# Optimization experiments

Measured on AMD Instinct MI355X. Metric: run time of the kernel, lower is better.

## Reference

```python
import jax, jax.numpy as jnp
import numpy as np

B, N, C = 2, 2048, 1024
H = 16
D = C // H  # head_dim = 64

def setup_inputs() -> dict:
    key = jax.random.key(0)
    ks = jax.random.split(key, 5)
    scale = 1.0 / np.sqrt(C)
    return {
        "x": jax.random.normal(ks[0], (B, N, C), dtype=jnp.float32),
        "w_qkv": jax.random.normal(ks[1], (C, 3 * C), dtype=jnp.float32) * scale,
        "b_qkv": jnp.zeros((3 * C,), dtype=jnp.float32),
        "w_out": jax.random.normal(ks[2], (C, C), dtype=jnp.float32) * scale,
        "b_out": jnp.zeros((C,), dtype=jnp.float32),
    }

def reference(x, w_qkv, b_qkv, w_out, b_out):
    b, n, c = x.shape
    # fused QKV projection: [B,N,3C] -> [3,B,H,N,D]
    qkv = (x @ w_qkv + b_qkv).reshape(b, n, 3, H, D).transpose(2, 0, 3, 1, 4)
    q, k, v = qkv[0], qkv[1], qkv[2]
    # scaled dot-product attention (dropout is identity in eval / p=0)
    attn = jnp.einsum('bhqd,bhkd->bhqk', q, k) * (D ** -0.5)
    attn = jax.nn.softmax(attn, axis=-1)
    out = jnp.einsum('bhqk,bhkd->bhqd', attn, v)
    out = out.transpose(0, 2, 1, 3).reshape(b, n, c)
    return out @ w_out + b_out
```

## Files before the change

### kernel.cpp

```cpp
#include <hip/hip_runtime.h>

typedef unsigned short u16;
typedef __bf16 bf16x8 __attribute__((ext_vector_type(8)));
typedef __bf16 bf16x4 __attribute__((ext_vector_type(4)));
typedef float f32x4 __attribute__((ext_vector_type(4)));

#define LOG2E 1.44269504088896340736f

constexpr int Bc = 2, Nc = 2048, Cch = 1024, Hh = 16, Dd = 64;
constexpr int Mrows = Bc * Nc;
constexpr int N_QKV = 3 * Cch;

__device__ __forceinline__ u16 f2bf(float f) {
  unsigned int u = __float_as_uint(f);
  u += 0x7fffu + ((u >> 16) & 1u);
  return (u16)(u >> 16);
}

__device__ __forceinline__ void gload16(const void* g, void* l) {
  __builtin_amdgcn_global_load_lds((const __attribute__((address_space(1))) void*)g,
                                   (__attribute__((address_space(3))) void*)l, 16, 0, 0);
}

#define MFMA(a, b, c) __builtin_amdgcn_mfma_f32_16x16x32_bf16(a, b, c, 0, 0, 0)

__global__ __launch_bounds__(256) void cast_x_kernel(const float* __restrict__ in,
                                                     u16* __restrict__ out, int n4) {
  int i = blockIdx.x * 256 + threadIdx.x;
  if (i >= n4) return;
  float4 v = *(const float4*)&in[i * 4];
  union { u16 h[4]; short4 s; } u;
  u.h[0] = f2bf(v.x); u.h[1] = f2bf(v.y); u.h[2] = f2bf(v.z); u.h[3] = f2bf(v.w);
  *(short4*)&out[i * 4] = u.s;
}

__global__ __launch_bounds__(256) void transpose_cast_kernel(const float* __restrict__ in,
                                                             u16* __restrict__ out,
                                                             int R, int Cq) {
  __shared__ float tile[32][33];
  int bx = blockIdx.x * 32;
  int by = blockIdx.y * 32;
  int tx = threadIdx.x & 31, ty = threadIdx.x >> 5;
#pragma unroll
  for (int i = 0; i < 32; i += 8)
    tile[ty + i][tx] = in[(size_t)(by + ty + i) * Cq + bx + tx];
  __syncthreads();
#pragma unroll
  for (int i = 0; i < 32; i += 8)
    out[(size_t)(bx + ty + i) * R + by + tx] = f2bf(tile[tx][ty + i]);
}

__global__ __launch_bounds__(256) void gemm_qkv_kernel(const u16* __restrict__ A,
                                                       const u16* __restrict__ Bt,
                                                       const float* __restrict__ bias,
                                                       u16* __restrict__ Qo,
                                                       u16* __restrict__ Ko,
                                                       u16* __restrict__ Vto) {
  __shared__ u16 As[128 * 32];
  __shared__ u16 Bs[128 * 32];
  f32x4 acc[4][4] = {};
  int tid = threadIdx.x, lane = tid & 63, wid = tid >> 6;
  int wr = wid >> 1, wc = wid & 1;
  int l15 = lane & 15, g = lane >> 4;
  int rowBase = blockIdx.x * 128, colBase = blockIdx.y * 128;
  int rowS = tid >> 2, c8 = (tid & 3) << 3;

  for (int k0 = 0; k0 < 1024; k0 += 32) {
    __syncthreads();
    gload16(&A[(size_t)(rowBase + rowS) * 1024 + k0 + c8],        (char*)As + wid * 1024);
    gload16(&A[(size_t)(rowBase + 64 + rowS) * 1024 + k0 + c8],   (char*)As + 4096 + wid * 1024);
    gload16(&Bt[(size_t)(colBase + rowS) * 1024 + k0 + c8],       (char*)Bs + wid * 1024);
    gload16(&Bt[(size_t)(colBase + 64 + rowS) * 1024 + k0 + c8],  (char*)Bs + 4096 + wid * 1024);
    __syncthreads();
    bf16x8 af[4], bfv[4];
#pragma unroll
    for (int m = 0; m < 4; ++m)
      af[m] = *(const bf16x8*)&As[(wr * 64 + m * 16 + l15) * 32 + g * 8];
#pragma unroll
    for (int n = 0; n < 4; ++n)
      bfv[n] = *(const bf16x8*)&Bs[(wc * 64 + n * 16 + l15) * 32 + g * 8];
#pragma unroll
    for (int m = 0; m < 4; ++m)
#pragma unroll
      for (int n = 0; n < 4; ++n)
        acc[m][n] = MFMA(af[m], bfv[n], acc[m][n]);
  }

#pragma unroll
  for (int m = 0; m < 4; ++m)
#pragma unroll
    for (int n = 0; n < 4; ++n) {
      int colc = colBase + wc * 64 + n * 16 + l15;
      float bv = bias[colc];
      int s = colc >> 10, hd = colc & 1023;
      int h = hd >> 6, d = hd & 63;
      float scale = (s == 0) ? 0.125f : 1.0f;
#pragma unroll
      for (int j = 0; j < 4; ++j) {
        int r = rowBase + wr * 64 + m * 16 + g * 4 + j;
        int b = r >> 11, nn = r & 2047;
        u16 v = f2bf((acc[m][n][j] + bv) * scale);
        size_t bh = (size_t)(b * 16 + h);
        if (s == 0)      Qo[(bh * 2048 + nn) * 64 + d] = v;
        else if (s == 1) Ko[(bh * 2048 + nn) * 64 + d] = v;
        else             Vto[(bh * 64 + d) * 2048 + nn] = v;
      }
    }
}

__global__ __launch_bounds__(256) void attn_kernel(const u16* __restrict__ Q,
                                                   const u16* __restrict__ Km,
                                                   const u16* __restrict__ Vt,
                                                   u16* __restrict__ AO) {
  __shared__ u16 Ks[64 * 72];
  __shared__ u16 Vs[64 * 72];
  __shared__ u16 Ps[128 * 72];
  int tid = threadIdx.x, lane = tid & 63, w = tid >> 6;
  int l15 = lane & 15, g = lane >> 4;
  int bidw = (blockIdx.x & 7) * 64 + (blockIdx.x >> 3);
  int bh = bidw >> 4, qt = bidw & 15;
  int b = bh >> 4, h = bh & 15;
  const size_t base = (size_t)bh * 2048 * 64;
  int qrow0 = qt * 128 + w * 32;

  bf16x8 qf[2][2];
#pragma unroll
  for (int mm = 0; mm < 2; ++mm)
#pragma unroll
    for (int ks = 0; ks < 2; ++ks)
      qf[mm][ks] = *(const bf16x8*)&Q[base + (size_t)(qrow0 + mm * 16 + l15) * 64 + ks * 32 + g * 8];

  f32x4 o[2][4] = {};
  float m_run[2] = {-1e30f, -1e30f};
  float l_run[2] = {0.f, 0.f};

  for (int nk0 = 0; nk0 < 2048; nk0 += 64) {
#pragma unroll
    for (int it = 0; it < 2; ++it) {
      int c = tid + it * 256;
      int rr = c >> 3, cc = (c & 7) * 8;
      *(int4*)&Ks[rr * 72 + cc] = *(const int4*)&Km[base + (size_t)(nk0 + rr) * 64 + cc];
      *(int4*)&Vs[rr * 72 + cc] = *(const int4*)&Vt[base + (size_t)rr * 2048 + nk0 + cc];
    }
    __syncthreads();

    f32x4 st[2][4] = {};
#pragma unroll
    for (int ks = 0; ks < 2; ++ks) {
      bf16x8 kf[4];
#pragma unroll
      for (int n = 0; n < 4; ++n)
        kf[n] = *(const bf16x8*)&Ks[(n * 16 + l15) * 72 + ks * 32 + g * 8];
#pragma unroll
      for (int mm = 0; mm < 2; ++mm)
#pragma unroll
        for (int n = 0; n < 4; ++n)
          st[mm][n] = MFMA(kf[n], qf[mm][ks], st[mm][n]);
    }

#pragma unroll
    for (int mm = 0; mm < 2; ++mm) {
      f32x4 mx;
#pragma unroll
      for (int j = 0; j < 4; ++j)
        mx[j] = fmaxf(fmaxf(st[mm][0][j], st[mm][1][j]), fmaxf(st[mm][2][j], st[mm][3][j]));
      float mloc = fmaxf(fmaxf(mx[0], mx[1]), fmaxf(mx[2], mx[3]));
      mloc = fmaxf(mloc, __shfl_xor(mloc, 16));
      mloc = fmaxf(mloc, __shfl_xor(mloc, 32));
      float mold = m_run[mm];
      float mnew = fmaxf(mold, mloc);
      float alpha = exp2f((mold - mnew) * LOG2E);
      m_run[mm] = mnew;
      float c = mnew * LOG2E;
      f32x4 sum4 = {0.f, 0.f, 0.f, 0.f};
#pragma unroll
      for (int n = 0; n < 4; ++n) {
#pragma unroll
        for (int j = 0; j < 4; ++j)
          st[mm][n][j] = exp2f(fmaf(st[mm][n][j], LOG2E, -c));
        sum4 += st[mm][n];
      }
      float rs = (sum4[0] + sum4[1]) + (sum4[2] + sum4[3]);
      rs += __shfl_xor(rs, 16);
      rs += __shfl_xor(rs, 32);
      l_run[mm] = l_run[mm] * alpha + rs;
#pragma unroll
      for (int dn = 0; dn < 4; ++dn) o[mm][dn] *= alpha;
#pragma unroll
      for (int n = 0; n < 4; ++n) {
        bf16x4 pv;
#pragma unroll
        for (int j = 0; j < 4; ++j) pv[j] = (__bf16)st[mm][n][j];
        *(bf16x4*)&Ps[(w * 32 + mm * 16 + l15) * 72 + n * 16 + g * 4] = pv;
      }
    }

#pragma unroll
    for (int ks = 0; ks < 2; ++ks) {
      bf16x8 pf[2];
#pragma unroll
      for (int mm = 0; mm < 2; ++mm)
        pf[mm] = *(const bf16x8*)&Ps[(w * 32 + mm * 16 + l15) * 72 + ks * 32 + g * 8];
#pragma unroll
      for (int dn = 0; dn < 4; ++dn) {
        bf16x8 vf = *(const bf16x8*)&Vs[(dn * 16 + l15) * 72 + ks * 32 + g * 8];
#pragma unroll
        for (int mm = 0; mm < 2; ++mm)
          o[mm][dn] = MFMA(vf, pf[mm], o[mm][dn]);
      }
    }
    __syncthreads();
  }

#pragma unroll
  for (int mm = 0; mm < 2; ++mm) {
    float inv = 1.0f / l_run[mm];
    int nq = qrow0 + mm * 16 + l15;
    size_t rowb = ((size_t)b * 2048 + nq) * 1024 + h * 64;
#pragma unroll
    for (int dn = 0; dn < 4; ++dn) {
      bf16x4 ov;
#pragma unroll
      for (int j = 0; j < 4; ++j) ov[j] = (__bf16)(o[mm][dn][j] * inv);
      *(bf16x4*)&AO[rowb + dn * 16 + g * 4] = ov;
    }
  }
}

__global__ __launch_bounds__(256) void gemm_proj_kernel(const u16* __restrict__ A,
                                                        const u16* __restrict__ Bt,
                                                        const float* __restrict__ bias,
                                                        float* __restrict__ out) {
  __shared__ u16 As[128 * 32];
  __shared__ u16 Bs[128 * 32];
  f32x4 acc[4][4] = {};
  int tid = threadIdx.x, lane = tid & 63, wid = tid >> 6;
  int wr = wid >> 1, wc = wid & 1;
  int l15 = lane & 15, g = lane >> 4;
  int rowBase = blockIdx.x * 128, colBase = blockIdx.y * 128;
  int rowS = tid >> 2, c8 = (tid & 3) << 3;

  for (int k0 = 0; k0 < 1024; k0 += 32) {
    __syncthreads();
    gload16(&A[(size_t)(rowBase + rowS) * 1024 + k0 + c8],        (char*)As + wid * 1024);
    gload16(&A[(size_t)(rowBase + 64 + rowS) * 1024 + k0 + c8],   (char*)As + 4096 + wid * 1024);
    gload16(&Bt[(size_t)(colBase + rowS) * 1024 + k0 + c8],       (char*)Bs + wid * 1024);
    gload16(&Bt[(size_t)(colBase + 64 + rowS) * 1024 + k0 + c8],  (char*)Bs + 4096 + wid * 1024);
    __syncthreads();
    bf16x8 af[4], bfv[4];
#pragma unroll
    for (int m = 0; m < 4; ++m)
      af[m] = *(const bf16x8*)&As[(wr * 64 + m * 16 + l15) * 32 + g * 8];
#pragma unroll
    for (int n = 0; n < 4; ++n)
      bfv[n] = *(const bf16x8*)&Bs[(wc * 64 + n * 16 + l15) * 32 + g * 8];
#pragma unroll
    for (int m = 0; m < 4; ++m)
#pragma unroll
      for (int n = 0; n < 4; ++n)
        acc[m][n] = MFMA(af[m], bfv[n], acc[m][n]);
  }

#pragma unroll
  for (int m = 0; m < 4; ++m)
#pragma unroll
    for (int n = 0; n < 4; ++n) {
      int colc = colBase + wc * 64 + n * 16 + l15;
      float bv = bias[colc];
#pragma unroll
      for (int j = 0; j < 4; ++j) {
        int r = rowBase + wr * 64 + m * 16 + g * 4 + j;
        out[(size_t)r * 1024 + colc] = acc[m][n][j] + bv;
      }
    }
}

extern "C" void kernel_launch(void* const* d_in, const int* in_sizes, int n_in,
                              void* d_out, int out_size, void* d_ws, size_t ws_size,
                              hipStream_t stream) {
  const float* x     = (const float*)d_in[0];
  const float* w_qkv = (const float*)d_in[1];
  const float* b_qkv = (const float*)d_in[2];
  const float* w_out = (const float*)d_in[3];
  const float* b_out = (const float*)d_in[4];
  float* out = (float*)d_out;

  char* w = (char*)d_ws;
  u16* Xb  = (u16*)(w);
  u16* W1T = (u16*)(w + (8u << 20));
  u16* W2T = (u16*)(w + (14u << 20));
  u16* Qb  = (u16*)(w + (16u << 20));
  u16* Kb  = (u16*)(w + (24u << 20));
  u16* Vtb = (u16*)(w + (32u << 20));
  u16* AO  = (u16*)(w + (40u << 20));

  cast_x_kernel<<<4096, 256, 0, stream>>>(x, Xb, Mrows * Cch / 4);
  transpose_cast_kernel<<<dim3(N_QKV / 32, Cch / 32), 256, 0, stream>>>(w_qkv, W1T, Cch, N_QKV);
  transpose_cast_kernel<<<dim3(Cch / 32, Cch / 32), 256, 0, stream>>>(w_out, W2T, Cch, Cch);
  gemm_qkv_kernel<<<dim3(Mrows / 128, N_QKV / 128), 256, 0, stream>>>(Xb, W1T, b_qkv, Qb, Kb, Vtb);
  attn_kernel<<<512, 256, 0, stream>>>(Qb, Kb, Vtb, AO);
  gemm_proj_kernel<<<dim3(Mrows / 128, Cch / 128), 256, 0, stream>>>(AO, W2T, b_out, out);

  (void)in_sizes; (void)n_in; (void)out_size; (void)ws_size;
}
```

Measured before the change: 234.4 us.

## Halve attention query tile, fold log2e into Q, remap GEMM blocks per XCD

The attention kernel now gives each block 64 query rows, 16 per wave, so the grid grows to 1024 blocks and per-wave registers and LDS for P shrink. The price is that each K/V tile loaded into LDS is reused by half as many queries. The log2(e) factor moves into the Q scale in the QKV GEMM epilogue, which removes per-element multiplies from the softmax exp2 computation. Both GEMMs switch to a 1D grid with an XCD-aware block remap, meant to improve L2 locality across the chiplets.

```diff
diff --git a/kernel.cpp b/kernel.cpp
--- a/kernel.cpp
+++ b/kernel.cpp
@@ -50,6 +50,7 @@
     out[(size_t)(bx + ty + i) * R + by + tx] = f2bf(tile[tx][ty + i]);
 }
 
+template <int NWG, int NY>
 __global__ __launch_bounds__(256) void gemm_qkv_kernel(const u16* __restrict__ A,
                                                        const u16* __restrict__ Bt,
                                                        const float* __restrict__ bias,
@@ -62,7 +63,8 @@
   int tid = threadIdx.x, lane = tid & 63, wid = tid >> 6;
   int wr = wid >> 1, wc = wid & 1;
   int l15 = lane & 15, g = lane >> 4;
-  int rowBase = blockIdx.x * 128, colBase = blockIdx.y * 128;
+  int wgid = (blockIdx.x & 7) * (NWG >> 3) + (blockIdx.x >> 3);
+  int rowBase = (wgid / NY) * 128, colBase = (wgid % NY) * 128;
   int rowS = tid >> 2, c8 = (tid & 3) << 3;
 
   for (int k0 = 0; k0 < 1024; k0 += 32) {
@@ -94,7 +96,7 @@
       float bv = bias[colc];
       int s = colc >> 10, hd = colc & 1023;
       int h = hd >> 6, d = hd & 63;
-      float scale = (s == 0) ? 0.125f : 1.0f;
+      float scale = (s == 0) ? (0.125f * LOG2E) : 1.0f;
 #pragma unroll
       for (int j = 0; j < 4; ++j) {
         int r = rowBase + wr * 64 + m * 16 + g * 4 + j;
@@ -114,25 +116,23 @@
                                                    u16* __restrict__ AO) {
   __shared__ u16 Ks[64 * 72];
   __shared__ u16 Vs[64 * 72];
-  __shared__ u16 Ps[128 * 72];
+  __shared__ u16 Ps[64 * 72];
   int tid = threadIdx.x, lane = tid & 63, w = tid >> 6;
   int l15 = lane & 15, g = lane >> 4;
-  int bidw = (blockIdx.x & 7) * 64 + (blockIdx.x >> 3);
-  int bh = bidw >> 4, qt = bidw & 15;
+  int bidw = (blockIdx.x & 7) * 128 + (blockIdx.x >> 3);
+  int bh = bidw >> 5, qt = bidw & 31;
   int b = bh >> 4, h = bh & 15;
   const size_t base = (size_t)bh * 2048 * 64;
-  int qrow0 = qt * 128 + w * 32;
-
-  bf16x8 qf[2][2];
-#pragma unroll
-  for (int mm = 0; mm < 2; ++mm)
-#pragma unroll
-    for (int ks = 0; ks < 2; ++ks)
-      qf[mm][ks] = *(const bf16x8*)&Q[base + (size_t)(qrow0 + mm * 16 + l15) * 64 + ks * 32 + g * 8];
-
-  f32x4 o[2][4] = {};
-  float m_run[2] = {-1e30f, -1e30f};
-  float l_run[2] = {0.f, 0.f};
+  int qrow0 = qt * 64 + w * 16;
+
+  bf16x8 qf[2];
+#pragma unroll
+  for (int ks = 0; ks < 2; ++ks)
+    qf[ks] = *(const bf16x8*)&Q[base + (size_t)(qrow0 + l15) * 64 + ks * 32 + g * 8];
+
+  f32x4 o[4] = {};
+  float m_run = -1e30f;
+  float l_run = 0.f;
 
   for (int nk0 = 0; nk0 < 2048; nk0 += 64) {
 #pragma unroll
@@ -144,7 +144,7 @@
     }
     __syncthreads();
 
-    f32x4 st[2][4] = {};
+    f32x4 st[4] = {};
 #pragma unroll
     for (int ks = 0; ks < 2; ++ks) {
       bf16x8 kf[4];
@@ -152,81 +152,68 @@
       for (int n = 0; n < 4; ++n)
         kf[n] = *(const bf16x8*)&Ks[(n * 16 + l15) * 72 + ks * 32 + g * 8];
 #pragma unroll
-      for (int mm = 0; mm < 2; ++mm)
-#pragma unroll
-        for (int n = 0; n < 4; ++n)
-          st[mm][n] = MFMA(kf[n], qf[mm][ks], st[mm][n]);
-    }
-
-#pragma unroll
-    for (int mm = 0; mm < 2; ++mm) {
-      f32x4 mx;
+      for (int n = 0; n < 4; ++n)
+        st[n] = MFMA(kf[n], qf[ks], st[n]);
+    }
+
+    f32x4 mx;
+#pragma unroll
+    for (int j = 0; j < 4; ++j)
+      mx[j] = fmaxf(fmaxf(st[0][j], st[1][j]), fmaxf(st[2][j], st[3][j]));
+    float mloc = fmaxf(fmaxf(mx[0], mx[1]), fmaxf(mx[2], mx[3]));
+    mloc = fmaxf(mloc, __shfl_xor(mloc, 16));
+    mloc = fmaxf(mloc, __shfl_xor(mloc, 32));
+    float mold = m_run;
+    float mnew = fmaxf(mold, mloc);
+    float alpha = exp2f(mold - mnew);
+    m_run = mnew;
+    f32x4 sum4 = {0.f, 0.f, 0.f, 0.f};
+#pragma unroll
+    for (int n = 0; n < 4; ++n) {
 #pragma unroll
       for (int j = 0; j < 4; ++j)
-        mx[j] = fmaxf(fmaxf(st[mm][0][j], st[mm][1][j]), fmaxf(st[mm][2][j], st[mm][3][j]));
-      float mloc = fmaxf(fmaxf(mx[0], mx[1]), fmaxf(mx[2], mx[3]));
-      mloc = fmaxf(mloc, __shfl_xor(mloc, 16));
-      mloc = fmaxf(mloc, __shfl_xor(mloc, 32));
-      float mold = m_run[mm];
-      float mnew = fmaxf(mold, mloc);
-      float alpha = exp2f((mold - mnew) * LOG2E);
-      m_run[mm] = mnew;
-      float c = mnew * LOG2E;
-      f32x4 sum4 = {0.f, 0.f, 0.f, 0.f};
-#pragma unroll
-      for (int n = 0; n < 4; ++n) {
-#pragma unroll
-        for (int j = 0; j < 4; ++j)
-          st[mm][n][j] = exp2f(fmaf(st[mm][n][j], LOG2E, -c));
-        sum4 += st[mm][n];
-      }
-      float rs = (sum4[0] + sum4[1]) + (sum4[2] + sum4[3]);
-      rs += __shfl_xor(rs, 16);
-      rs += __shfl_xor(rs, 32);
-      l_run[mm] = l_run[mm] * alpha + rs;
-#pragma unroll
-      for (int dn = 0; dn < 4; ++dn) o[mm][dn] *= alpha;
-#pragma unroll
-      for (int n = 0; n < 4; ++n) {
-        bf16x4 pv;
-#pragma unroll
-        for (int j = 0; j < 4; ++j) pv[j] = (__bf16)st[mm][n][j];
-        *(bf16x4*)&Ps[(w * 32 + mm * 16 + l15) * 72 + n * 16 + g * 4] = pv;
-      }
+        st[n][j] = exp2f(st[n][j] - mnew);
+      sum4 += st[n];
+    }
+    float rs = (sum4[0] + sum4[1]) + (sum4[2] + sum4[3]);
+    rs += __shfl_xor(rs, 16);
+    rs += __shfl_xor(rs, 32);
+    l_run = l_run * alpha + rs;
+#pragma unroll
+    for (int dn = 0; dn < 4; ++dn) o[dn] *= alpha;
+#pragma unroll
+    for (int n = 0; n < 4; ++n) {
+      bf16x4 pv;
+#pragma unroll
+      for (int j = 0; j < 4; ++j) pv[j] = (__bf16)st[n][j];
+      *(bf16x4*)&Ps[(w * 16 + l15) * 72 + n * 16 + g * 4] = pv;
     }
 
 #pragma unroll
     for (int ks = 0; ks < 2; ++ks) {
-      bf16x8 pf[2];
-#pragma unroll
-      for (int mm = 0; mm < 2; ++mm)
-        pf[mm] = *(const bf16x8*)&Ps[(w * 32 + mm * 16 + l15) * 72 + ks * 32 + g * 8];
+      bf16x8 pf = *(const bf16x8*)&Ps[(w * 16 + l15) * 72 + ks * 32 + g * 8];
 #pragma unroll
       for (int dn = 0; dn < 4; ++dn) {
         bf16x8 vf = *(const bf16x8*)&Vs[(dn * 16 + l15) * 72 + ks * 32 + g * 8];
-#pragma unroll
-        for (int mm = 0; mm < 2; ++mm)
-          o[mm][dn] = MFMA(vf, pf[mm], o[mm][dn]);
+        o[dn] = MFMA(vf, pf, o[dn]);
       }
     }
     __syncthreads();
   }
 
-#pragma unroll
-  for (int mm = 0; mm < 2; ++mm) {
-    float inv = 1.0f / l_run[mm];
-    int nq = qrow0 + mm * 16 + l15;
-    size_t rowb = ((size_t)b * 2048 + nq) * 1024 + h * 64;
-#pragma unroll
-    for (int dn = 0; dn < 4; ++dn) {
-      bf16x4 ov;
-#pragma unroll
-      for (int j = 0; j < 4; ++j) ov[j] = (__bf16)(o[mm][dn][j] * inv);
-      *(bf16x4*)&AO[rowb + dn * 16 + g * 4] = ov;
-    }
-  }
-}
-
+  float inv = 1.0f / l_run;
+  int nq = qrow0 + l15;
+  size_t rowb = ((size_t)b * 2048 + nq) * 1024 + h * 64;
+#pragma unroll
+  for (int dn = 0; dn < 4; ++dn) {
+    bf16x4 ov;
+#pragma unroll
+    for (int j = 0; j < 4; ++j) ov[j] = (__bf16)(o[dn][j] * inv);
+    *(bf16x4*)&AO[rowb + dn * 16 + g * 4] = ov;
+  }
+}
+
+template <int NWG, int NY>
 __global__ __launch_bounds__(256) void gemm_proj_kernel(const u16* __restrict__ A,
                                                         const u16* __restrict__ Bt,
                                                         const float* __restrict__ bias,
@@ -237,7 +224,8 @@
   int tid = threadIdx.x, lane = tid & 63, wid = tid >> 6;
   int wr = wid >> 1, wc = wid & 1;
   int l15 = lane & 15, g = lane >> 4;
-  int rowBase = blockIdx.x * 128, colBase = blockIdx.y * 128;
+  int wgid = (blockIdx.x & 7) * (NWG >> 3) + (blockIdx.x >> 3);
+  int rowBase = (wgid / NY) * 128, colBase = (wgid % NY) * 128;
   int rowS = tid >> 2, c8 = (tid & 3) << 3;
 
   for (int k0 = 0; k0 < 1024; k0 += 32) {
@@ -297,9 +285,9 @@
   cast_x_kernel<<<4096, 256, 0, stream>>>(x, Xb, Mrows * Cch / 4);
   transpose_cast_kernel<<<dim3(N_QKV / 32, Cch / 32), 256, 0, stream>>>(w_qkv, W1T, Cch, N_QKV);
   transpose_cast_kernel<<<dim3(Cch / 32, Cch / 32), 256, 0, stream>>>(w_out, W2T, Cch, Cch);
-  gemm_qkv_kernel<<<dim3(Mrows / 128, N_QKV / 128), 256, 0, stream>>>(Xb, W1T, b_qkv, Qb, Kb, Vtb);
-  attn_kernel<<<512, 256, 0, stream>>>(Qb, Kb, Vtb, AO);
-  gemm_proj_kernel<<<dim3(Mrows / 128, Cch / 128), 256, 0, stream>>>(AO, W2T, b_out, out);
+  gemm_qkv_kernel<768, 24><<<768, 256, 0, stream>>>(Xb, W1T, b_qkv, Qb, Kb, Vtb);
+  attn_kernel<<<1024, 256, 0, stream>>>(Qb, Kb, Vtb, AO);
+  gemm_proj_kernel<256, 8><<<256, 256, 0, stream>>>(AO, W2T, b_out, out);
 
   (void)in_sizes; (void)n_in; (void)out_size; (void)ws_size;
 }
```

After: 239.2 us. 2.0% more time.

## Double-buffer attention K/V loads with async LDS copies and lazy softmax rescale

Applied to the files above, without the earlier changes.

The attention kernel now stages K and V tiles through double-buffered LDS using direct global-to-LDS loads with an XOR swizzle, so the next tile's fetch overlaps the current tile's compute. The log2e factor is folded into the Q scale, and the running-max rescale of the output and row sum is skipped unless a new max exceeds the old one by a threshold. Both GEMMs switch to a 1D grid with an XCD-aware workgroup remap so that neighbouring tiles share cache. The lazy rescale depends on fp32 headroom, and the loop still issues one redundant prefetch after the last tile.

```diff
diff --git a/kernel.cpp b/kernel.cpp
--- a/kernel.cpp
+++ b/kernel.cpp
@@ -50,6 +50,7 @@
     out[(size_t)(bx + ty + i) * R + by + tx] = f2bf(tile[tx][ty + i]);
 }
 
+template <int NWG, int NY>
 __global__ __launch_bounds__(256) void gemm_qkv_kernel(const u16* __restrict__ A,
                                                        const u16* __restrict__ Bt,
                                                        const float* __restrict__ bias,
@@ -62,7 +63,8 @@
   int tid = threadIdx.x, lane = tid & 63, wid = tid >> 6;
   int wr = wid >> 1, wc = wid & 1;
   int l15 = lane & 15, g = lane >> 4;
-  int rowBase = blockIdx.x * 128, colBase = blockIdx.y * 128;
+  int wgid = (blockIdx.x & 7) * (NWG >> 3) + (blockIdx.x >> 3);
+  int rowBase = (wgid / NY) * 128, colBase = (wgid % NY) * 128;
   int rowS = tid >> 2, c8 = (tid & 3) << 3;
 
   for (int k0 = 0; k0 < 1024; k0 += 32) {
@@ -94,7 +96,7 @@
       float bv = bias[colc];
       int s = colc >> 10, hd = colc & 1023;
       int h = hd >> 6, d = hd & 63;
-      float scale = (s == 0) ? 0.125f : 1.0f;
+      float scale = (s == 0) ? (0.125f * LOG2E) : 1.0f;
 #pragma unroll
       for (int j = 0; j < 4; ++j) {
         int r = rowBase + wr * 64 + m * 16 + g * 4 + j;
@@ -112,15 +114,19 @@
                                                    const u16* __restrict__ Km,
                                                    const u16* __restrict__ Vt,
                                                    u16* __restrict__ AO) {
-  __shared__ u16 Ks[64 * 72];
-  __shared__ u16 Vs[64 * 72];
+  __shared__ u16 KV[16384];
   __shared__ u16 Ps[128 * 72];
   int tid = threadIdx.x, lane = tid & 63, w = tid >> 6;
   int l15 = lane & 15, g = lane >> 4;
-  int bidw = (blockIdx.x & 7) * 64 + (blockIdx.x >> 3);
+  int r8 = lane >> 3;
+  int src_col = (((lane & 7) ^ (r8 & 7)) << 4);
+  int r7q = l15 & 7;
+  int bidw = ((blockIdx.x & 7) << 6) + (blockIdx.x >> 3);
   int bh = bidw >> 4, qt = bidw & 15;
   int b = bh >> 4, h = bh & 15;
   const size_t base = (size_t)bh * 2048 * 64;
+  const char* Kg = (const char*)(Km + base);
+  const char* Vg = (const char*)(Vt + base);
   int qrow0 = qt * 128 + w * 32;
 
   bf16x8 qf[2][2];
@@ -129,20 +135,38 @@
 #pragma unroll
     for (int ks = 0; ks < 2; ++ks)
       qf[mm][ks] = *(const bf16x8*)&Q[base + (size_t)(qrow0 + mm * 16 + l15) * 64 + ks * 32 + g * 8];
+
+#define STAGE(cb, nk)                                                          \
+  do {                                                                         \
+    int kr = (nk) + w * 8 + r8;                                                \
+    gload16(Kg + (size_t)kr * 128 + src_col,                                   \
+            (char*)KV + (cb) * 8192 + w * 1024);                               \
+    gload16(Kg + (size_t)(kr + 32) * 128 + src_col,                            \
+            (char*)KV + (cb) * 8192 + 4096 + w * 1024);                        \
+    int vr = w * 8 + r8;                                                       \
+    gload16(Vg + (size_t)vr * 4096 + (nk) * 2 + src_col,                       \
+            (char*)KV + 16384 + (cb) * 8192 + w * 1024);                       \
+    gload16(Vg + (size_t)(vr + 32) * 4096 + (nk) * 2 + src_col,                \
+            (char*)KV + 16384 + (cb) * 8192 + 4096 + w * 1024);                \
+  } while (0)
 
   f32x4 o[2][4] = {};
   float m_run[2] = {-1e30f, -1e30f};
   float l_run[2] = {0.f, 0.f};
-
-  for (int nk0 = 0; nk0 < 2048; nk0 += 64) {
-#pragma unroll
-    for (int it = 0; it < 2; ++it) {
-      int c = tid + it * 256;
-      int rr = c >> 3, cc = (c & 7) * 8;
-      *(int4*)&Ks[rr * 72 + cc] = *(const int4*)&Km[base + (size_t)(nk0 + rr) * 64 + cc];
-      *(int4*)&Vs[rr * 72 + cc] = *(const int4*)&Vt[base + (size_t)rr * 2048 + nk0 + cc];
-    }
-    __syncthreads();
+  int xk[2] = {((0 + g) ^ r7q) << 4, ((4 + g) ^ r7q) << 4};
+
+  STAGE(0, 0);
+
+  for (int t = 0; t < 32; ++t) {
+    int cur = t & 1;
+    int nk_next = ((t + 1) & 31) * 64;
+    STAGE(cur ^ 1, nk_next);
+    asm volatile("s_waitcnt vmcnt(4)" ::: "memory");
+    __builtin_amdgcn_s_barrier();
+    asm volatile("" ::: "memory");
+
+    const char* bK = (const char*)KV + cur * 8192;
+    const char* bV = (const char*)KV + 16384 + cur * 8192;
 
     f32x4 st[2][4] = {};
 #pragma unroll
@@ -150,7 +174,7 @@
       bf16x8 kf[4];
 #pragma unroll
       for (int n = 0; n < 4; ++n)
-        kf[n] = *(const bf16x8*)&Ks[(n * 16 + l15) * 72 + ks * 32 + g * 8];
+        kf[n] = *(const bf16x8*)(bK + (n * 16 + l15) * 128 + xk[ks]);
 #pragma unroll
       for (int mm = 0; mm < 2; ++mm)
 #pragma unroll
@@ -158,6 +182,7 @@
           st[mm][n] = MFMA(kf[n], qf[mm][ks], st[mm][n]);
     }
 
+    float pm[2];
 #pragma unroll
     for (int mm = 0; mm < 2; ++mm) {
       f32x4 mx;
@@ -167,25 +192,33 @@
       float mloc = fmaxf(fmaxf(mx[0], mx[1]), fmaxf(mx[2], mx[3]));
       mloc = fmaxf(mloc, __shfl_xor(mloc, 16));
       mloc = fmaxf(mloc, __shfl_xor(mloc, 32));
-      float mold = m_run[mm];
-      float mnew = fmaxf(mold, mloc);
-      float alpha = exp2f((mold - mnew) * LOG2E);
-      m_run[mm] = mnew;
-      float c = mnew * LOG2E;
+      pm[mm] = mloc;
+    }
+    if (__any((pm[0] > m_run[0] + 8.f) || (pm[1] > m_run[1] + 8.f))) {
+#pragma unroll
+      for (int mm = 0; mm < 2; ++mm) {
+        float mnew = fmaxf(m_run[mm], pm[mm]);
+        float alpha = exp2f(m_run[mm] - mnew);
+        m_run[mm] = mnew;
+        l_run[mm] *= alpha;
+#pragma unroll
+        for (int dn = 0; dn < 4; ++dn) o[mm][dn] *= alpha;
+      }
+    }
+#pragma unroll
+    for (int mm = 0; mm < 2; ++mm) {
       f32x4 sum4 = {0.f, 0.f, 0.f, 0.f};
 #pragma unroll
       for (int n = 0; n < 4; ++n) {
 #pragma unroll
         for (int j = 0; j < 4; ++j)
-          st[mm][n][j] = exp2f(fmaf(st[mm][n][j], LOG2E, -c));
+          st[mm][n][j] = exp2f(st[mm][n][j] - m_run[mm]);
         sum4 += st[mm][n];
       }
       float rs = (sum4[0] + sum4[1]) + (sum4[2] + sum4[3]);
       rs += __shfl_xor(rs, 16);
       rs += __shfl_xor(rs, 32);
-      l_run[mm] = l_run[mm] * alpha + rs;
-#pragma unroll
-      for (int dn = 0; dn < 4; ++dn) o[mm][dn] *= alpha;
+      l_run[mm] += rs;
 #pragma unroll
       for (int n = 0; n < 4; ++n) {
         bf16x4 pv;
@@ -203,14 +236,16 @@
         pf[mm] = *(const bf16x8*)&Ps[(w * 32 + mm * 16 + l15) * 72 + ks * 32 + g * 8];
 #pragma unroll
       for (int dn = 0; dn < 4; ++dn) {
-        bf16x8 vf = *(const bf16x8*)&Vs[(dn * 16 + l15) * 72 + ks * 32 + g * 8];
+        bf16x8 vf = *(const bf16x8*)(bV + (dn * 16 + l15) * 128 + xk[ks]);
 #pragma unroll
         for (int mm = 0; mm < 2; ++mm)
           o[mm][dn] = MFMA(vf, pf[mm], o[mm][dn]);
       }
     }
-    __syncthreads();
+    asm volatile("" ::: "memory");
+    __builtin_amdgcn_s_barrier();
   }
+#undef STAGE
 
 #pragma unroll
   for (int mm = 0; mm < 2; ++mm) {
@@ -227,6 +262,7 @@
   }
 }
 
+template <int NWG, int NY>
 __global__ __launch_bounds__(256) void gemm_proj_kernel(const u16* __restrict__ A,
                                                         const u16* __restrict__ Bt,
                                                         const float* __restrict__ bias,
@@ -237,7 +273,8 @@
   int tid = threadIdx.x, lane = tid & 63, wid = tid >> 6;
   int wr = wid >> 1, wc = wid & 1;
   int l15 = lane & 15, g = lane >> 4;
-  int rowBase = blockIdx.x * 128, colBase = blockIdx.y * 128;
+  int wgid = (blockIdx.x & 7) * (NWG >> 3) + (blockIdx.x >> 3);
+  int rowBase = (wgid / NY) * 128, colBase = (wgid % NY) * 128;
   int rowS = tid >> 2, c8 = (tid & 3) << 3;
 
   for (int k0 = 0; k0 < 1024; k0 += 32) {
@@ -297,9 +334,9 @@
   cast_x_kernel<<<4096, 256, 0, stream>>>(x, Xb, Mrows * Cch / 4);
   transpose_cast_kernel<<<dim3(N_QKV / 32, Cch / 32), 256, 0, stream>>>(w_qkv, W1T, Cch, N_QKV);
   transpose_cast_kernel<<<dim3(Cch / 32, Cch / 32), 256, 0, stream>>>(w_out, W2T, Cch, Cch);
-  gemm_qkv_kernel<<<dim3(Mrows / 128, N_QKV / 128), 256, 0, stream>>>(Xb, W1T, b_qkv, Qb, Kb, Vtb);
+  gemm_qkv_kernel<768, 24><<<768, 256, 0, stream>>>(Xb, W1T, b_qkv, Qb, Kb, Vtb);
   attn_kernel<<<512, 256, 0, stream>>>(Qb, Kb, Vtb, AO);
-  gemm_proj_kernel<<<dim3(Mrows / 128, Cch / 128), 256, 0, stream>>>(AO, W2T, b_out, out);
+  gemm_proj_kernel<256, 8><<<256, 256, 0, stream>>>(AO, W2T, b_out, out);
 
   (void)in_sizes; (void)n_in; (void)out_size; (void)ws_size;
 }
```

After: 224.5 us. 4.2% less time.
